# Kernel optimization log

Hardware: AMD Instinct MI355X
Metric: run time of the kernel (lower is better)

Reference implementation:

```python
import jax, jax.numpy as jnp
import numpy as np


def setup_inputs() -> dict:
    key = jax.random.key(0)
    k1, k2, k3, k4 = jax.random.split(key, 4)
    T, H, E, I = 4096, 1024, 8, 3584
    return {
        "hidden_states": jax.random.normal(k1, (T, H), dtype=jnp.float32),
        "gate_w": jax.random.normal(k2, (H, E), dtype=jnp.float32) * 0.02,
        "w1": jax.random.normal(k3, (E, H, I), dtype=jnp.float32) * 0.02,
        "w2": jax.random.normal(k4, (E, I, H), dtype=jnp.float32) * 0.02,
        "top_k": 2,
    }


def reference(hidden_states, gate_w, w1, w2, top_k):
    # Router: logits -> softmax -> top-k -> renormalize (Mixtral / vLLM fused_moe)
    router_logits = hidden_states @ gate_w                    # [T, E]
    probs = jax.nn.softmax(router_logits, axis=-1)
    top_vals, top_idx = jax.lax.top_k(probs, top_k)           # [T, K]
    top_vals = top_vals / jnp.sum(top_vals, axis=-1, keepdims=True)
    E = gate_w.shape[1]
    # Dense per-(token, expert) combine weights, zero for non-selected experts
    dense_w = jnp.sum(jax.nn.one_hot(top_idx, E, dtype=hidden_states.dtype)
                      * top_vals[..., None], axis=1)          # [T, E]
    # Expert MLP: silu(x @ w1[e]) @ w2[e], weighted by routing probs
    act = jax.nn.silu(jnp.einsum('th,ehi->tei', hidden_states, w1))  # [T, E, I]
    act = act * dense_w[:, :, None]
    out = jnp.einsum('tei,eih->th', act, w2)                  # [T, H]
    return out
```

## Files before the change

### kernel.cpp

```cpp
#include <hip/hip_runtime.h>
#include <hip/hip_bf16.h>

#define T_TOK 4096
#define H_DIM 1024
#define E_NUM 8
#define I_DIM 3584
#define NPAIR (T_TOK * 2)
#define MAX_RT 72

#define BM 128
#define BN 128
#define BK 64
#define G0_NWG (MAX_RT * (I_DIM / BN))
#define WT_NB 3584

typedef __attribute__((ext_vector_type(8))) short bf16x8;
typedef __attribute__((ext_vector_type(4))) float f32x4;
typedef __attribute__((ext_vector_type(8))) unsigned short ushort8_t;
typedef __attribute__((ext_vector_type(4))) unsigned short ushort4_t;

__device__ __forceinline__ unsigned short f2bf(float x) {
  unsigned int u = __float_as_uint(x);
  unsigned int r = (u + 0x7FFFu + ((u >> 16) & 1u)) >> 16;
  return (unsigned short)r;
}

__device__ __forceinline__ void gload16(const void* g, unsigned short* l) {
  __builtin_amdgcn_global_load_lds(
      (const __attribute__((address_space(1))) void*)g,
      (__attribute__((address_space(3))) void*)l, 16, 0, 0);
}

__device__ __forceinline__ void transpose_body2(const float* __restrict__ src,
                                                unsigned short* __restrict__ dst,
                                                int R, int C, int e, int c0, int r0,
                                                char* smem) {
  float (*tile)[65] = reinterpret_cast<float (*)[65]>(smem);
  const float* s = src + (size_t)e * R * C;
  unsigned short* d = dst + (size_t)e * R * C;
  const int th = threadIdx.x;
  const int tr = th >> 4;
  const int tc4 = (th & 15) * 4;
  const int wc = th >> 3;
  const int wr = (th & 7) * 8;
  ushort8_t oA[2];
#pragma unroll
  for (int it = 0; it < 4; ++it) {
    const int r = it * 16 + tr;
    float4 v = *reinterpret_cast<const float4*>(s + (size_t)(r0 + r) * C + c0 + tc4);
    tile[r][tc4] = v.x; tile[r][tc4 + 1] = v.y; tile[r][tc4 + 2] = v.z; tile[r][tc4 + 3] = v.w;
  }
  __syncthreads();
#pragma unroll
  for (int it = 0; it < 2; ++it) {
    const int c = it * 32 + wc;
#pragma unroll
    for (int j = 0; j < 8; ++j) oA[it][j] = f2bf(tile[wr + j][c]);
  }
  __syncthreads();
#pragma unroll
  for (int it = 0; it < 4; ++it) {
    const int r = it * 16 + tr;
    float4 v = *reinterpret_cast<const float4*>(s + (size_t)(r0 + 64 + r) * C + c0 + tc4);
    tile[r][tc4] = v.x; tile[r][tc4 + 1] = v.y; tile[r][tc4 + 2] = v.z; tile[r][tc4 + 3] = v.w;
  }
  __syncthreads();
#pragma unroll
  for (int it = 0; it < 2; ++it) {
    const int c = it * 32 + wc;
    ushort8_t oB;
#pragma unroll
    for (int j = 0; j < 8; ++j) oB[j] = f2bf(tile[wr + j][c]);
    *reinterpret_cast<ushort8_t*>(d + (size_t)(c0 + c) * R + r0 + wr) = oA[it];
    *reinterpret_cast<ushort8_t*>(d + (size_t)(c0 + c) * R + r0 + 64 + wr) = oB;
  }
}

__device__ __forceinline__ void router_body(const float* __restrict__ hs,
                                            const float* __restrict__ gw,
                                            unsigned short* __restrict__ hsb,
                                            int* __restrict__ eid, float* __restrict__ wgt,
                                            int* __restrict__ counts, int rbid, char* smem) {
  float* s_gw = reinterpret_cast<float*>(smem);
  int* s_cnt = reinterpret_cast<int*>(smem + 32768);
  const int th = threadIdx.x;
  for (int u = th; u < 2048; u += 256) {
    const f32x4 v = *reinterpret_cast<const f32x4*>(gw + u * 4);
    *reinterpret_cast<f32x4*>(&s_gw[(u ^ ((u >> 3) & 7)) * 4]) = v;
  }
  if (th < E_NUM) s_cnt[th] = 0;
  __syncthreads();

  const int l = th & 63, w = th >> 6;
#pragma unroll 1
  for (int tt = 0; tt < 4; ++tt) {
    const int t = rbid * 16 + w * 4 + tt;
    const float* hrow = hs + (size_t)t * H_DIM;
    unsigned short* brow = hsb + (size_t)t * H_DIM;
    float acc[E_NUM];
#pragma unroll
    for (int e = 0; e < E_NUM; ++e) acc[e] = 0.f;
#pragma unroll
    for (int i = 0; i < 4; ++i) {
      const int h0 = i * 256 + l * 4;
      const f32x4 x = *reinterpret_cast<const f32x4*>(hrow + h0);
      ushort4_t o = { f2bf(x[0]), f2bf(x[1]), f2bf(x[2]), f2bf(x[3]) };
      *reinterpret_cast<ushort4_t*>(brow + h0) = o;
#pragma unroll
      for (int j = 0; j < 4; ++j) {
        const int h = h0 + j;
        const int p0 = (h * 2) ^ ((h >> 2) & 7);
        const f32x4 g0 = *reinterpret_cast<const f32x4*>(&s_gw[p0 * 4]);
        const f32x4 g1 = *reinterpret_cast<const f32x4*>(&s_gw[(p0 ^ 1) * 4]);
        acc[0] += x[j] * g0[0]; acc[1] += x[j] * g0[1];
        acc[2] += x[j] * g0[2]; acc[3] += x[j] * g0[3];
        acc[4] += x[j] * g1[0]; acc[5] += x[j] * g1[1];
        acc[6] += x[j] * g1[2]; acc[7] += x[j] * g1[3];
      }
    }
#pragma unroll
    for (int e = 0; e < E_NUM; ++e) {
#pragma unroll
      for (int off = 1; off < 64; off <<= 1) acc[e] += __shfl_xor(acc[e], off);
    }
    if (l == 0) {
      int i1 = 0;
#pragma unroll
      for (int e = 1; e < E_NUM; ++e) if (acc[e] > acc[i1]) i1 = e;
      int i2 = (i1 == 0) ? 1 : 0;
#pragma unroll
      for (int e = 0; e < E_NUM; ++e) if (e != i1 && acc[e] > acc[i2]) i2 = e;
      const float e2 = __expf(acc[i2] - acc[i1]);
      const float inv = 1.f / (1.f + e2);
      eid[t * 2] = i1;     wgt[t * 2] = inv;
      eid[t * 2 + 1] = i2; wgt[t * 2 + 1] = e2 * inv;
      atomicAdd(&s_cnt[i1], 1);
      atomicAdd(&s_cnt[i2], 1);
    }
  }
  __syncthreads();
  if (th < E_NUM && s_cnt[th] > 0) atomicAdd(&counts[th], s_cnt[th]);
}

__global__ __launch_bounds__(256) void prep1_kernel(
    const float* __restrict__ w1, const float* __restrict__ hs,
    const float* __restrict__ gw,
    unsigned short* __restrict__ w1t, unsigned short* __restrict__ hsb,
    int* __restrict__ eid, float* __restrict__ wgt, int* __restrict__ counts) {
  __shared__ char smem[33024];
  const int bid = blockIdx.x;
  if (bid < 256) {
    router_body(hs, gw, hsb, eid, wgt, counts, bid, smem);
    return;
  }
  const int idx = bid - 256;
  const int e = idx / 448, rem = idx % 448;
  transpose_body2(w1, w1t, H_DIM, I_DIM, e, (rem % 56) * 64, (rem / 56) * 128, smem);
}

__global__ void scatter_kernel(const int* __restrict__ eid, const int* __restrict__ counts,
                               int* __restrict__ fill, int* __restrict__ rowmap,
                               int* __restrict__ posmap) {
  __shared__ int hist[E_NUM], base[E_NUM];
  const int th = threadIdx.x;
  const int p = blockIdx.x * 256 + th;
  if (th < E_NUM) hist[th] = 0;
  __syncthreads();
  const int e = eid[p];
  const int rloc = atomicAdd(&hist[e], 1);
  __syncthreads();
  if (th < E_NUM) base[th] = (hist[th] > 0) ? atomicAdd(&fill[th], hist[th]) : 0;
  __syncthreads();
  int off = 0;
#pragma unroll
  for (int i = 0; i < E_NUM; ++i) off += (i < e) ? counts[i] : 0;
  const int pos = off + base[e] + rloc;
  rowmap[pos] = p;
  posmap[p] = pos;
}

__global__ void combine_kernel(const float* __restrict__ res, const int* __restrict__ posmap,
                               float* __restrict__ out) {
  const int t = blockIdx.x;
  const int th = threadIdx.x;
  const int a = posmap[t * 2];
  const int b = posmap[t * 2 + 1];
  const float4 va = *reinterpret_cast<const float4*>(res + (size_t)a * H_DIM + th * 4);
  const float4 vb = *reinterpret_cast<const float4*>(res + (size_t)b * H_DIM + th * 4);
  float4 o = { va.x + vb.x, va.y + vb.y, va.z + vb.z, va.w + vb.w };
  *reinterpret_cast<float4*>(out + (size_t)t * H_DIM + th * 4) = o;
}

__global__ __launch_bounds__(256, 4) void gemm0_w2t_kernel(
    const unsigned short* __restrict__ hsb, const unsigned short* __restrict__ w1t,
    unsigned short* __restrict__ act,
    const float* __restrict__ w2, unsigned short* __restrict__ w2t,
    const int* __restrict__ counts, const int* __restrict__ rowmap) {
  __shared__ char smem[(BM * BK + BN * BK) * 2];
  const int bid = blockIdx.x;
  if (bid >= G0_NWG) {
    const int idx = bid - G0_NWG;
    const int e = idx / 448, rem = idx % 448;
    transpose_body2(w2, w2t, I_DIM, H_DIM, e, (rem % 16) * 64, (rem / 16) * 128, smem);
    return;
  }
  unsigned short* As = reinterpret_cast<unsigned short*>(smem);
  unsigned short* Bs = As + BM * BK;

  constexpr int CHUNK = G0_NWG / 8;
  const int wgid = (bid & 7) * CHUNK + (bid >> 3);
  const int l = wgid % CHUNK;
  const int sg = l / 36;
  const int q = l % 36;
  const int rt = (wgid / CHUNK) * 9 + q % 9;
  const int ct = sg * 4 + q / 9;

  int e = -1, loc_rt = 0, off_e = 0, cnt = 0;
  {
    int acc_t = 0, off = 0;
#pragma unroll
    for (int ee = 0; ee < E_NUM; ++ee) {
      const int c = counts[ee];
      const int nt = (c + BM - 1) >> 7;
      if (e < 0 && rt < acc_t + nt) { e = ee; loc_rt = rt - acc_t; off_e = off; cnt = c; }
      acc_t += nt; off += c;
    }
  }
  if (e < 0) return;

  const int cnt_local = min(BM, cnt - loc_rt * BM);
  const int r_base = off_e + loc_rt * BM;
  const int th = threadIdx.x;
  const int lane = th & 63, wid = th >> 6;

  const int n0 = ct * BN;
  const unsigned short* wbase = w1t + (size_t)e * ((size_t)I_DIM * H_DIM) + (size_t)n0 * H_DIM;

  const int srow = lane >> 3;
  const int cg = (lane & 7) ^ srow;
  const char* aptr[4];
  const char* bptr[4];
#pragma unroll
  for (int i = 0; i < 4; ++i) {
    const int r = i * 32 + wid * 8 + srow;
    const int rr = (r < cnt_local) ? r : (cnt_local - 1);
    const int tok = rowmap[off_e + loc_rt * BM + rr] >> 1;
    aptr[i] = (const char*)(hsb + (size_t)tok * H_DIM) + cg * 16;
    bptr[i] = (const char*)(wbase + (size_t)r * H_DIM) + cg * 16;
  }
  unsigned short* dstA[4];
  unsigned short* dstB[4];
#pragma unroll
  for (int i = 0; i < 4; ++i) {
    dstA[i] = &As[(i * 32 + wid * 8) * BK];
    dstB[i] = &Bs[(i * 32 + wid * 8) * BK];
  }

  f32x4 acc[4][4];
#pragma unroll
  for (int m = 0; m < 4; ++m)
#pragma unroll
    for (int n = 0; n < 4; ++n) acc[m][n] = (f32x4){0.f, 0.f, 0.f, 0.f};

  const int wm = (wid >> 1) * 64;
  const int wn = (wid & 1) * 64;
  const int fr = lane & 15;
  const int fq = lane >> 4;
  const int sxor = fr & 7;

  for (int k0 = 0; k0 < H_DIM; k0 += BK) {
    const int kb = k0 * 2;
#pragma unroll
    for (int i = 0; i < 4; ++i) gload16(aptr[i] + kb, dstA[i]);
#pragma unroll
    for (int i = 0; i < 4; ++i) gload16(bptr[i] + kb, dstB[i]);
    __syncthreads();

#pragma unroll
    for (int kk = 0; kk < 2; ++kk) {
      bf16x8 af[4], bf[4];
#pragma unroll
      for (int m = 0; m < 4; ++m)
        af[m] = *reinterpret_cast<const bf16x8*>(
            &As[(wm + m * 16 + fr) * BK + ((kk * 4 + fq) ^ sxor) * 8]);
#pragma unroll
      for (int n = 0; n < 4; ++n)
        bf[n] = *reinterpret_cast<const bf16x8*>(
            &Bs[(wn + n * 16 + fr) * BK + ((kk * 4 + fq) ^ sxor) * 8]);
#pragma unroll
      for (int m = 0; m < 4; ++m)
#pragma unroll
        for (int n = 0; n < 4; ++n)
          acc[m][n] = __builtin_amdgcn_mfma_f32_16x16x32_bf16(af[m], bf[n], acc[m][n], 0, 0, 0);
    }
    __syncthreads();
  }

#pragma unroll
  for (int m = 0; m < 4; ++m) {
    const int row = wm + m * 16 + fq * 4;
#pragma unroll
    for (int n = 0; n < 4; ++n) {
      const int col = wn + n * 16 + fr;
#pragma unroll
      for (int r = 0; r < 4; ++r) {
        const int rw = row + r;
        if (rw < cnt_local) {
          const float x = acc[m][n][r];
          const float s = x / (1.f + __expf(-x));
          act[(size_t)(r_base + rw) * I_DIM + n0 + col] = f2bf(s);
        }
      }
    }
  }
}

__launch_bounds__(256, 4)
__global__ void moe_gemm1(const unsigned short* __restrict__ w2t,
                          const unsigned short* __restrict__ act_in,
                          float* __restrict__ res,
                          const int* __restrict__ counts,
                          const int* __restrict__ rowmap,
                          const float* __restrict__ wgt) {
  constexpr int NCT = H_DIM / BN;
  constexpr int NWG = MAX_RT * NCT;
  constexpr int CHUNK = NWG / 8;

  __shared__ unsigned short As[BM * BK];
  __shared__ unsigned short Bs[BN * BK];
  __shared__ float s_w[BM];

  const int bid = blockIdx.x;
  const int wgid = (bid & 7) * CHUNK + (bid >> 3);
  int rt, ct;
  {
    const int c9 = (wgid / CHUNK) * 9;
    const int l = wgid % CHUNK;
    if (l < 64) {
      const int band = l >> 4, inner = l & 15;
      rt = c9 + band * 2 + (inner & 1);
      ct = inner >> 1;
    } else {
      rt = c9 + 8;
      ct = l - 64;
    }
  }

  int e = -1, loc_rt = 0, off_e = 0, cnt = 0;
  {
    int acc_t = 0, off = 0;
#pragma unroll
    for (int ee = 0; ee < E_NUM; ++ee) {
      const int c = counts[ee];
      const int nt = (c + BM - 1) >> 7;
      if (e < 0 && rt < acc_t + nt) { e = ee; loc_rt = rt - acc_t; off_e = off; cnt = c; }
      acc_t += nt; off += c;
    }
  }
  if (e < 0) return;

  const int cnt_local = min(BM, cnt - loc_rt * BM);
  const int r_base = off_e + loc_rt * BM;
  const int th = threadIdx.x;
  const int lane = th & 63, wid = th >> 6;

  if (th < BM) {
    int r = loc_rt * BM + th;
    if (r >= cnt) r = cnt - 1;
    s_w[th] = wgt[rowmap[off_e + r]];
  }

  const int n0 = ct * BN;
  const unsigned short* wbase = w2t + (size_t)e * ((size_t)I_DIM * H_DIM) + (size_t)n0 * I_DIM;

  const int srow = lane >> 3;
  const int cg = (lane & 7) ^ srow;
  const char* aptr[4];
  const char* bptr[4];
#pragma unroll
  for (int i = 0; i < 4; ++i) {
    const int r = i * 32 + wid * 8 + srow;
    const int rr = (r < cnt_local) ? r : (cnt_local - 1);
    aptr[i] = (const char*)(act_in + (size_t)(r_base + rr) * I_DIM) + cg * 16;
    bptr[i] = (const char*)(wbase + (size_t)r * I_DIM) + cg * 16;
  }
  unsigned short* dstA[4];
  unsigned short* dstB[4];
#pragma unroll
  for (int i = 0; i < 4; ++i) {
    dstA[i] = &As[(i * 32 + wid * 8) * BK];
    dstB[i] = &Bs[(i * 32 + wid * 8) * BK];
  }

  f32x4 acc[4][4];
#pragma unroll
  for (int m = 0; m < 4; ++m)
#pragma unroll
    for (int n = 0; n < 4; ++n) acc[m][n] = (f32x4){0.f, 0.f, 0.f, 0.f};

  const int wm = (wid >> 1) * 64;
  const int wn = (wid & 1) * 64;
  const int fr = lane & 15;
  const int fq = lane >> 4;
  const int sxor = fr & 7;

  for (int k0 = 0; k0 < I_DIM; k0 += BK) {
    const int kb = k0 * 2;
#pragma unroll
    for (int i = 0; i < 4; ++i) gload16(aptr[i] + kb, dstA[i]);
#pragma unroll
    for (int i = 0; i < 4; ++i) gload16(bptr[i] + kb, dstB[i]);
    __syncthreads();

#pragma unroll
    for (int kk = 0; kk < 2; ++kk) {
      bf16x8 af[4], bf[4];
#pragma unroll
      for (int m = 0; m < 4; ++m)
        af[m] = *reinterpret_cast<const bf16x8*>(
            &As[(wm + m * 16 + fr) * BK + ((kk * 4 + fq) ^ sxor) * 8]);
#pragma unroll
      for (int n = 0; n < 4; ++n)
        bf[n] = *reinterpret_cast<const bf16x8*>(
            &Bs[(wn + n * 16 + fr) * BK + ((kk * 4 + fq) ^ sxor) * 8]);
#pragma unroll
      for (int m = 0; m < 4; ++m)
#pragma unroll
        for (int n = 0; n < 4; ++n)
          acc[m][n] = __builtin_amdgcn_mfma_f32_16x16x32_bf16(af[m], bf[n], acc[m][n], 0, 0, 0);
    }
    __syncthreads();
  }

#pragma unroll
  for (int m = 0; m < 4; ++m) {
    const int row = wm + m * 16 + fq * 4;
#pragma unroll
    for (int n = 0; n < 4; ++n) {
      const int col = wn + n * 16 + fr;
#pragma unroll
      for (int r = 0; r < 4; ++r) {
        const int rw = row + r;
        if (rw < cnt_local)
          res[(size_t)(r_base + rw) * H_DIM + n0 + col] = acc[m][n][r] * s_w[rw];
      }
    }
  }
}

extern "C" void kernel_launch(void* const* d_in, const int* in_sizes, int n_in,
                              void* d_out, int out_size, void* d_ws, size_t ws_size,
                              hipStream_t stream) {
  const float* hs = (const float*)d_in[0];
  const float* gw = (const float*)d_in[1];
  const float* w1 = (const float*)d_in[2];
  const float* w2 = (const float*)d_in[3];
  float* out = (float*)d_out;

  char* ws = (char*)d_ws;
  const size_t WMAT = (size_t)E_NUM * I_DIM * H_DIM * 2;
  unsigned short* w1t = (unsigned short*)ws;
  unsigned short* w2t = (unsigned short*)(ws + WMAT);
  unsigned short* act = (unsigned short*)(ws + 2 * WMAT);
  unsigned short* hsb = (unsigned short*)(ws + 3 * WMAT);
  float* res = (float*)w1t;
  char* small = ws + 3 * WMAT + (size_t)T_TOK * H_DIM * 2;
  int* eid = (int*)small;
  float* wgt = (float*)(small + NPAIR * 4);
  int* rowmap = (int*)(small + 2 * NPAIR * 4);
  int* posmap = (int*)(small + 3 * NPAIR * 4);
  int* counts = (int*)(small + 4 * NPAIR * 4);
  int* fill = counts + 8;

  hipMemsetAsync(counts, 0, 16 * sizeof(int), stream);

  prep1_kernel<<<256 + WT_NB, 256, 0, stream>>>(w1, hs, gw, w1t, hsb, eid, wgt, counts);
  scatter_kernel<<<NPAIR / 256, 256, 0, stream>>>(eid, counts, fill, rowmap, posmap);

  gemm0_w2t_kernel<<<G0_NWG + WT_NB, 256, 0, stream>>>(
      hsb, w1t, act, w2, w2t, counts, rowmap);
  moe_gemm1<<<MAX_RT * (H_DIM / BN), 256, 0, stream>>>(
      w2t, act, res, counts, rowmap, wgt);

  combine_kernel<<<T_TOK, 256, 0, stream>>>(res, posmap, out);
}
```

Baseline: 244.6 us.

## Fuse combine into gemm1 via atomic adds and interleave transpose blocks with gemm0

Removes the separate combine kernel and posmap: moe_gemm1 now scales each row by its routing weight and atomically adds it into the zeroed output at the token row. The output is cleared with a memset. gemm0 block indexing is reworked so w2 transpose blocks are interleaved with GEMM blocks rather than appended at the end, which spreads bandwidth-bound and compute-bound work across the launch. This trades the intermediate result buffer and extra kernel for global atomics and an extra memset.

```diff
diff --git a/kernel.cpp b/kernel.cpp
--- a/kernel.cpp
+++ b/kernel.cpp
@@ -159,8 +159,7 @@
 }
 
 __global__ void scatter_kernel(const int* __restrict__ eid, const int* __restrict__ counts,
-                               int* __restrict__ fill, int* __restrict__ rowmap,
-                               int* __restrict__ posmap) {
+                               int* __restrict__ fill, int* __restrict__ rowmap) {
   __shared__ int hist[E_NUM], base[E_NUM];
   const int th = threadIdx.x;
   const int p = blockIdx.x * 256 + th;
@@ -174,21 +173,7 @@
   int off = 0;
 #pragma unroll
   for (int i = 0; i < E_NUM; ++i) off += (i < e) ? counts[i] : 0;
-  const int pos = off + base[e] + rloc;
-  rowmap[pos] = p;
-  posmap[p] = pos;
-}
-
-__global__ void combine_kernel(const float* __restrict__ res, const int* __restrict__ posmap,
-                               float* __restrict__ out) {
-  const int t = blockIdx.x;
-  const int th = threadIdx.x;
-  const int a = posmap[t * 2];
-  const int b = posmap[t * 2 + 1];
-  const float4 va = *reinterpret_cast<const float4*>(res + (size_t)a * H_DIM + th * 4);
-  const float4 vb = *reinterpret_cast<const float4*>(res + (size_t)b * H_DIM + th * 4);
-  float4 o = { va.x + vb.x, va.y + vb.y, va.z + vb.z, va.w + vb.w };
-  *reinterpret_cast<float4*>(out + (size_t)t * H_DIM + th * 4) = o;
+  rowmap[off + base[e] + rloc] = p;
 }
 
 __global__ __launch_bounds__(256, 4) void gemm0_w2t_kernel(
@@ -198,17 +183,22 @@
     const int* __restrict__ counts, const int* __restrict__ rowmap) {
   __shared__ char smem[(BM * BK + BN * BK) * 2];
   const int bid = blockIdx.x;
-  if (bid >= G0_NWG) {
-    const int idx = bid - G0_NWG;
+  const int oct = bid >> 3, l8 = bid & 7;
+  const int grp = oct / 25, pos = oct % 25;
+
+  if (pos >= 9) {
+    const int idx = (grp * 16 + (pos - 9)) * 8 + l8;
     const int e = idx / 448, rem = idx % 448;
     transpose_body2(w2, w2t, I_DIM, H_DIM, e, (rem % 16) * 64, (rem / 16) * 128, smem);
     return;
   }
+  const int g0idx = (grp * 9 + pos) * 8 + l8;
+
   unsigned short* As = reinterpret_cast<unsigned short*>(smem);
   unsigned short* Bs = As + BM * BK;
 
   constexpr int CHUNK = G0_NWG / 8;
-  const int wgid = (bid & 7) * CHUNK + (bid >> 3);
+  const int wgid = (g0idx & 7) * CHUNK + (g0idx >> 3);
   const int l = wgid % CHUNK;
   const int sg = l / 36;
   const int q = l % 36;
@@ -318,7 +308,7 @@
 __launch_bounds__(256, 4)
 __global__ void moe_gemm1(const unsigned short* __restrict__ w2t,
                           const unsigned short* __restrict__ act_in,
-                          float* __restrict__ res,
+                          float* __restrict__ out,
                           const int* __restrict__ counts,
                           const int* __restrict__ rowmap,
                           const float* __restrict__ wgt) {
@@ -328,6 +318,7 @@
 
   __shared__ unsigned short As[BM * BK];
   __shared__ unsigned short Bs[BN * BK];
+  __shared__ int s_pair[BM];
   __shared__ float s_w[BM];
 
   const int bid = blockIdx.x;
@@ -367,7 +358,9 @@
   if (th < BM) {
     int r = loc_rt * BM + th;
     if (r >= cnt) r = cnt - 1;
-    s_w[th] = wgt[rowmap[off_e + r]];
+    const int p = rowmap[off_e + r];
+    s_pair[th] = p;
+    s_w[th] = wgt[p];
   }
 
   const int n0 = ct * BN;
@@ -441,8 +434,10 @@
 #pragma unroll
       for (int r = 0; r < 4; ++r) {
         const int rw = row + r;
-        if (rw < cnt_local)
-          res[(size_t)(r_base + rw) * H_DIM + n0 + col] = acc[m][n][r] * s_w[rw];
+        if (rw < cnt_local) {
+          const int tok = s_pair[rw] >> 1;
+          atomicAdd(out + (size_t)tok * H_DIM + n0 + col, acc[m][n][r] * s_w[rw]);
+        }
       }
     }
   }
@@ -463,24 +458,21 @@
   unsigned short* w2t = (unsigned short*)(ws + WMAT);
   unsigned short* act = (unsigned short*)(ws + 2 * WMAT);
   unsigned short* hsb = (unsigned short*)(ws + 3 * WMAT);
-  float* res = (float*)w1t;
   char* small = ws + 3 * WMAT + (size_t)T_TOK * H_DIM * 2;
   int* eid = (int*)small;
   float* wgt = (float*)(small + NPAIR * 4);
   int* rowmap = (int*)(small + 2 * NPAIR * 4);
-  int* posmap = (int*)(small + 3 * NPAIR * 4);
-  int* counts = (int*)(small + 4 * NPAIR * 4);
+  int* counts = (int*)(small + 3 * NPAIR * 4);
   int* fill = counts + 8;
 
   hipMemsetAsync(counts, 0, 16 * sizeof(int), stream);
-
-  prep1_kernel<<<256 + WT_NB, 256, 0, stream>>>(w1, hs, gw, w1t, hsb, eid, wgt, counts);
-  scatter_kernel<<<NPAIR / 256, 256, 0, stream>>>(eid, counts, fill, rowmap, posmap);
+  hipMemsetAsync(d_out, 0, (size_t)T_TOK * H_DIM * sizeof(float), stream);
+
+  prep1_kernel<<<256 + 3584, 256, 0, stream>>>(w1, hs, gw, w1t, hsb, eid, wgt, counts);
+  scatter_kernel<<<NPAIR / 256, 256, 0, stream>>>(eid, counts, fill, rowmap);
 
   gemm0_w2t_kernel<<<G0_NWG + WT_NB, 256, 0, stream>>>(
       hsb, w1t, act, w2, w2t, counts, rowmap);
   moe_gemm1<<<MAX_RT * (H_DIM / BN), 256, 0, stream>>>(
-      w2t, act, res, counts, rowmap, wgt);
-
-  combine_kernel<<<T_TOK, 256, 0, stream>>>(res, posmap, out);
-}
+      w2t, act, out, counts, rowmap, wgt);
+}
```

Result: slower. 257.2 us (+5.1%).
